# Optimization experiments

Hardware: AMD Instinct MI355X
Metric: run time of the kernel (lower is better)

## Reference

```python
import jax, jax.numpy as jnp
import numpy as np

NUM_HEAD = 8
HEAD_SIZE = 32  # attention_size 256 / 8 heads


def setup_inputs() -> dict:
    key = jax.random.key(0)
    ks = jax.random.split(key, 10)
    B, S, H, A = 2, 4096, 256, 256
    x = jax.random.normal(ks[0], (B, S, H), dtype=jnp.float32)
    mask = jax.random.randint(ks[1], (B, S), 0, 2) > 0  # bool key-padding mask
    s = 0.02
    wq = jax.random.normal(ks[2], (A, H), dtype=jnp.float32) * s
    bq = jax.random.normal(ks[3], (A,), dtype=jnp.float32) * s
    wk = jax.random.normal(ks[4], (A, H), dtype=jnp.float32) * s
    bk = jax.random.normal(ks[5], (A,), dtype=jnp.float32) * s
    wv = jax.random.normal(ks[6], (A, H), dtype=jnp.float32) * s
    bv = jax.random.normal(ks[7], (A,), dtype=jnp.float32) * s
    wo = jax.random.normal(ks[8], (H, A), dtype=jnp.float32) * s
    bo = jax.random.normal(ks[9], (H,), dtype=jnp.float32) * s
    return {"x": x, "mask": mask, "wq": wq, "bq": bq, "wk": wk, "bk": bk,
            "wv": wv, "bv": bv, "wo": wo, "bo": bo}


def reference(x, mask, wq, bq, wk, bk, wv, bv, wo, bo):
    B, S, _ = x.shape
    # QKV projections -> [B, S, n_head, head_size]
    q = (x @ wq.T + bq).reshape(B, S, NUM_HEAD, HEAD_SIZE)
    k = (x @ wk.T + bk).reshape(B, S, NUM_HEAD, HEAD_SIZE)
    v = (x @ wv.T + bv).reshape(B, S, NUM_HEAD, HEAD_SIZE)
    # scores [B, H, Sq, Sk]
    attn = jnp.einsum('bqhd,bkhd->bhqk', q, k) / jnp.sqrt(
        jnp.asarray(HEAD_SIZE, dtype=x.dtype))
    # attn*mask - 1e5*~mask  ==  where(mask, attn, -1e5)
    attn = jnp.where(mask[:, None, None, :], attn, jnp.asarray(-100000.0, dtype=x.dtype))
    p = jax.nn.softmax(attn, axis=-1)
    o = jnp.einsum('bhqk,bkhd->bqhd', p, v).reshape(B, S, NUM_HEAD * HEAD_SIZE)
    return o @ wo.T + bo
```

## Files before the change

### kernel.cpp

```cpp
#include <hip/hip_runtime.h>

#define DEV __device__ __forceinline__

typedef __attribute__((ext_vector_type(8)))  short bf16x8;
typedef __attribute__((ext_vector_type(4)))  short s16x4;
typedef __attribute__((ext_vector_type(16))) float f32x16;

constexpr int SB = 2;
constexpr int SS = 4096;
constexpr int SH = 256;
constexpr int NHEAD = 8, HD = 32;
constexpr int M_TOK = SB * SS;
constexpr int NQKV = 3 * SH;

constexpr size_t OFF_CNT  = 0;
constexpr size_t OFF_BIAS = 256;
constexpr size_t OFF_XB   = OFF_BIAS + 32768;
constexpr size_t OFF_WQKV = OFF_XB + (size_t)M_TOK * SH * 2;
constexpr size_t OFF_BQKV = OFF_WQKV + (size_t)NQKV * SH * 2;
constexpr size_t OFF_WOB  = OFF_BQKV + 4096;
constexpr size_t OFF_BO   = OFF_WOB + (size_t)SH * SH * 2;
constexpr size_t OFF_Q    = OFF_BO + 1024;
constexpr size_t OFF_K    = OFF_Q + (size_t)M_TOK * SH * 2;
constexpr size_t OFF_V    = OFF_K + (size_t)M_TOK * SH * 2;
constexpr size_t OFF_VT   = OFF_V + (size_t)M_TOK * SH * 2;
constexpr size_t OFF_O    = OFF_VT + (size_t)M_TOK * SH * 2;
constexpr size_t WS_NEED  = OFF_O + (size_t)M_TOK * SH * 2;

DEV short f2bf(float f) {
  unsigned u = __builtin_bit_cast(unsigned, f);
  u = (u + 0x7FFFu + ((u >> 16) & 1u)) >> 16;
  return (short)u;
}

DEV float bf2f(short s) {
  return __builtin_bit_cast(float, ((unsigned)(unsigned short)s) << 16);
}

DEV float exp2_(float x) {
#if __has_builtin(__builtin_amdgcn_exp2f)
  return __builtin_amdgcn_exp2f(x);
#else
  float r;
  asm("v_exp_f32 %0, %1\n\ts_nop 0" : "=v"(r) : "v"(x));
  return r;
#endif
}

DEV unsigned cvtpk(float lo, float hi) {
  unsigned r;
  asm("v_cvt_pk_bf16_f32 %0, %1, %2" : "=v"(r) : "v"(lo), "v"(hi));
  return r;
}

DEV void plswap(unsigned& a, unsigned& b) {
  asm("v_permlane32_swap_b32 %0, %1" : "+v"(a), "+v"(b));
}

__global__ void prep_kernel(const float* __restrict__ x,
    const float* __restrict__ wq, const float* __restrict__ bq,
    const float* __restrict__ wk, const float* __restrict__ bk,
    const float* __restrict__ wv, const float* __restrict__ bv,
    const float* __restrict__ wo, const float* __restrict__ bo,
    short* __restrict__ xb, short* __restrict__ Wqkv, float* __restrict__ bqkv,
    short* __restrict__ wob, float* __restrict__ bof) {
  const float QS = (float)(1.4426950408889634 / 5.656854249492381);
  long i = ((long)blockIdx.x * 256 + threadIdx.x) * 8;
  const long NX = (long)M_TOK * SH;
  const long NW = (long)NQKV * SH;
  if (i < NX) {
    const float4* s = (const float4*)(x + i);
    float4 f0 = s[0], f1 = s[1];
    bf16x8 o;
    o[0]=f2bf(f0.x); o[1]=f2bf(f0.y); o[2]=f2bf(f0.z); o[3]=f2bf(f0.w);
    o[4]=f2bf(f1.x); o[5]=f2bf(f1.y); o[6]=f2bf(f1.z); o[7]=f2bf(f1.w);
    *(bf16x8*)(xb + i) = o;
    return;
  }
  i -= NX;
  if (i < NW) {
    int n = (int)(i >> 8), kk = (int)(i & 255);
    int tn = n >> 8, rr = n & 255;
    const float* src = (tn == 0 ? wq : (tn == 1 ? wk : wv)) + rr * 256 + kk;
    float sc = tn == 0 ? QS : 1.f;
    float4 f0 = *(const float4*)src, f1 = *(const float4*)(src + 4);
    bf16x8 o;
    o[0]=f2bf(f0.x*sc); o[1]=f2bf(f0.y*sc); o[2]=f2bf(f0.z*sc); o[3]=f2bf(f0.w*sc);
    o[4]=f2bf(f1.x*sc); o[5]=f2bf(f1.y*sc); o[6]=f2bf(f1.z*sc); o[7]=f2bf(f1.w*sc);
    *(bf16x8*)(Wqkv + i) = o;
    return;
  }
  i -= NW;
  if (i < NQKV) {
    int n = (int)i;
#pragma unroll
    for (int j = 0; j < 8; ++j) {
      int nn = n + j, tn = nn >> 8, rr = nn & 255;
      const float* src = tn == 0 ? bq : (tn == 1 ? bk : bv);
      bqkv[nn] = src[rr] * (tn == 0 ? QS : 1.f);
    }
    return;
  }
  i -= NQKV;
  if (i < (long)SH * SH) {
    const float4* s = (const float4*)(wo + i);
    float4 f0 = s[0], f1 = s[1];
    bf16x8 o;
    o[0]=f2bf(f0.x); o[1]=f2bf(f0.y); o[2]=f2bf(f0.z); o[3]=f2bf(f0.w);
    o[4]=f2bf(f1.x); o[5]=f2bf(f1.y); o[6]=f2bf(f1.z); o[7]=f2bf(f1.w);
    *(bf16x8*)(wob + i) = o;
    return;
  }
  i -= (long)SH * SH;
  if (i < SH) {
#pragma unroll
    for (int j = 0; j < 8; ++j) bof[i + j] = bo[i + j];
  }
}

template <int MODE>
__global__ __launch_bounds__(256) void gemm_kernel(
    const short* __restrict__ Ag, const short* __restrict__ Bg,
    const float* __restrict__ bias,
    short* __restrict__ q, short* __restrict__ k, short* __restrict__ v,
    float* __restrict__ outf) {
  __shared__ __align__(16) short lA[8192];
  __shared__ __align__(16) short lB[4096];
  const int tid = threadIdx.x;
  const int lane = tid & 63, w = tid >> 6;
  const int wm = w >> 1, wn = w & 1;
  const int hi = lane >> 5, l31 = lane & 31;
  const int mb = blockIdx.x, nb = blockIdx.y;
  f32x16 acc0, acc1;
#pragma unroll
  for (int i = 0; i < 16; ++i) { acc0[i] = 0.f; acc1[i] = 0.f; }
  bf16x8 ra[4], rb[2];
  const int am = tid >> 3, ak = tid & 7;
  auto gload = [&](int kb) {
#pragma unroll
    for (int p = 0; p < 4; ++p)
      ra[p] = *(const bf16x8*)(Ag + (size_t)(mb * 128 + p * 32 + am) * 256 + kb * 64 + ak * 8);
#pragma unroll
    for (int p = 0; p < 2; ++p)
      rb[p] = *(const bf16x8*)(Bg + (size_t)(nb * 64 + p * 32 + am) * 256 + kb * 64 + ak * 8);
  };
  gload(0);
  for (int kb = 0; kb < 4; ++kb) {
    __syncthreads();
#pragma unroll
    for (int p = 0; p < 4; ++p)
      *(bf16x8*)(lA + (ak * 128 + p * 32 + am) * 8) = ra[p];
#pragma unroll
    for (int p = 0; p < 2; ++p)
      *(bf16x8*)(lB + (ak * 64 + p * 32 + am) * 8) = rb[p];
    __syncthreads();
    if (kb < 3) gload(kb + 1);
#pragma unroll
    for (int ks = 0; ks < 4; ++ks) {
      bf16x8 af0 = *(const bf16x8*)(lA + ((2 * ks + hi) * 128 + wm * 64 + l31) * 8);
      bf16x8 af1 = *(const bf16x8*)(lA + ((2 * ks + hi) * 128 + wm * 64 + 32 + l31) * 8);
      bf16x8 bf  = *(const bf16x8*)(lB + ((2 * ks + hi) * 64 + wn * 32 + l31) * 8);
      acc0 = __builtin_amdgcn_mfma_f32_32x32x16_bf16(af0, bf, acc0, 0, 0, 0);
      acc1 = __builtin_amdgcn_mfma_f32_32x32x16_bf16(af1, bf, acc1, 0, 0, 0);
    }
  }
  const int ncol = nb * 64 + wn * 32 + l31;
  const float bval = bias[ncol];
  if (MODE == 0) {
    const int tensor = nb >> 2;
    short* dst = tensor == 0 ? q : (tensor == 1 ? k : v);
    const int a = (nb & 3) * 64 + wn * 32 + l31;
    const int hh = a >> 5, d = a & 31;
#pragma unroll
    for (int mt = 0; mt < 2; ++mt) {
      const f32x16& acc = mt == 0 ? acc0 : acc1;
#pragma unroll
      for (int r = 0; r < 16; ++r) {
        int gm = mb * 128 + wm * 64 + mt * 32 + (r & 3) + 8 * (r >> 2) + 4 * hi;
        int bb = gm >> 12, ss = gm & 4095;
        dst[(((size_t)bb * NHEAD + hh) * SS + ss) * HD + d] = f2bf(acc[r] + bval);
      }
    }
  } else {
#pragma unroll
    for (int mt = 0; mt < 2; ++mt) {
      const f32x16& acc = mt == 0 ? acc0 : acc1;
#pragma unroll
      for (int r = 0; r < 16; ++r) {
        int gm = mb * 128 + wm * 64 + mt * 32 + (r & 3) + 8 * (r >> 2) + 4 * hi;
        outf[(size_t)gm * SH + ncol] = acc[r] + bval;
      }
    }
  }
}

__global__ void scan_mask_kernel(const unsigned char* __restrict__ m,
                                 int* __restrict__ idxC, float* __restrict__ biasC,
                                 int* __restrict__ cnts) {
  __shared__ int f_mis, f_off4, f_3f;
  __shared__ int ts[256];
  const int tid = threadIdx.x, b = blockIdx.x;
  if (tid == 0) { f_mis = 0; f_off4 = 0; f_3f = 0; }
  __syncthreads();
  int lm = 0, lo4 = 0, l3f = 0;
  for (int i = tid; i < 8192; i += 256) {
    unsigned char c = m[i];
    if (c) {
      if (i & 3) lm = 1;
      if ((i & 7) == 4) lo4 = 1;
      if ((i & 3) == 3 && c == 0x3F) l3f = 1;
    }
  }
  if (lm)  atomicOr(&f_mis, 1);
  if (lo4) atomicOr(&f_off4, 1);
  if (l3f) atomicOr(&f_3f, 1);
  __syncthreads();
  const int f = !f_mis ? (f_off4 ? 1 : 3) : (f_3f ? 2 : 0);
  int bits = 0;
  const int rbase = b * 4096 + tid * 16;
#pragma unroll
  for (int j = 0; j < 16; ++j) {
    int r = rbase + j;
    bool on;
    if (f == 0)      on = m[r] != 0;
    else if (f == 1) on = m[(size_t)r * 4] != 0;
    else if (f == 2) on = m[(size_t)r * 4 + 3] != 0;
    else             on = m[(size_t)r * 8] != 0;
    bits |= (int)on << j;
  }
  const int cnt = __popc(bits);
  ts[tid] = cnt;
  __syncthreads();
  for (int off = 1; off < 256; off <<= 1) {
    int u = (tid >= off) ? ts[tid - off] : 0;
    __syncthreads();
    ts[tid] += u;
    __syncthreads();
  }
  const int total = ts[255];
  int pos = ts[tid] - cnt;
  int* idxB = idxC + b * 4096;
  float* biasB = biasC + b * 4096;
  if (total == 0) {
    for (int j = tid; j < 4096; j += 256) { idxB[j] = j; biasB[j] = 0.f; }
    if (tid == 0) cnts[b] = 4096;
    return;
  }
#pragma unroll
  for (int j = 0; j < 16; ++j)
    if ((bits >> j) & 1) { idxB[pos] = tid * 16 + j; biasB[pos] = 0.f; ++pos; }
  int cntpad = (total + 255) & ~255;
  if (cntpad < 256) cntpad = 256;
  for (int j = total + tid; j < cntpad; j += 256) { idxB[j] = -1; biasB[j] = -100000.f; }
  if (tid == 0) cnts[b] = cntpad;
}

__global__ __launch_bounds__(256) void gather_kv_kernel(const short* __restrict__ K,
    const short* __restrict__ V, const int* __restrict__ idxC, const int* __restrict__ cnts,
    short* __restrict__ Kc, short* __restrict__ Vt) {
  const int bh = blockIdx.y, b = bh >> 3;
  const int jb = blockIdx.x * 64;
  if (jb >= cnts[b]) return;
  __shared__ short t[64][33];
  const int tid = threadIdx.x;
  const int s = tid >> 2, g = tid & 3;
  const int ix = idxC[b * 4096 + jb + s];
  bf16x8 kvv{}, vvv{};
  if (ix >= 0) {
    kvv = *(const bf16x8*)(K + ((size_t)bh * SS + ix) * HD + g * 8);
    vvv = *(const bf16x8*)(V + ((size_t)bh * SS + ix) * HD + g * 8);
  }
  *(bf16x8*)(Kc + ((size_t)bh * SS + jb + s) * HD + g * 8) = kvv;
#pragma unroll
  for (int j = 0; j < 8; ++j) t[s][g * 8 + j] = vvv[j];
  __syncthreads();
  const int d = tid >> 3, gs = tid & 7;
  bf16x8 out;
#pragma unroll
  for (int j = 0; j < 8; ++j) out[j] = t[gs * 8 + j][d];
  *(bf16x8*)(Vt + ((size_t)bh * HD + d) * SS + jb + gs * 8) = out;
}

__global__ __launch_bounds__(256, 4) void attn_kernel(const short* __restrict__ Q,
    const short* __restrict__ Kc, const short* __restrict__ Vt,
    const float* __restrict__ biasC, const int* __restrict__ cnts,
    short* __restrict__ OP0, short* __restrict__ OP1, float* __restrict__ Lp) {
  __shared__ __align__(16) short sK[4096];
  __shared__ __align__(16) short sV[4096];
  __shared__ __align__(16) float sB[128];
  const int tid = threadIdx.x;
  const int lane = tid & 63, wave = tid >> 6;
  const int hi = lane >> 5, l31 = lane & 31;
  const int qblk = blockIdx.x, bh = blockIdx.y, half = blockIdx.z;
  const int b = bh >> 3, h = bh & 7;
  const int Lh = cnts[b] >> 1;
  const int NIT = Lh >> 7;
  const int kv0 = half * Lh;
  const short* Kb = Kc + ((size_t)bh * SS + kv0) * HD;
  const short* Vb = Vt + (size_t)bh * HD * SS + kv0;
  const float* biasB = biasC + b * SS + kv0;
  const int qbase = qblk * 128 + wave * 32;
  const short* Qrow = Q + ((size_t)bh * SS + qbase + l31) * HD;
  const bf16x8 qf0 = *(const bf16x8*)(Qrow + hi * 8);
  const bf16x8 qf1 = *(const bf16x8*)(Qrow + 16 + hi * 8);
  bf16x8 ones;
#pragma unroll
  for (int j = 0; j < 8; ++j) ones[j] = (short)0x3F80;
  f32x16 accO, lacc;
#pragma unroll
  for (int i = 0; i < 16; ++i) { accO[i] = 0.f; lacc[i] = 0.f; }
  const int kvs = tid >> 2, gd = tid & 3;
  const int dv = tid >> 3, gkv = tid & 7;
  const short* kvsrc = Kb + (size_t)kvs * HD + gd * 8;
  const short* vvsrc = Vb + (size_t)dv * SS + gkv * 8;
  short* kdst0 = sK + ((size_t)gd * 128 + kvs) * 8;
  short* kdst1 = sK + ((size_t)gd * 128 + 64 + kvs) * 8;
  short* vdst0 = sV + ((size_t)gkv * 32 + dv) * 8;
  short* vdst1 = sV + ((size_t)(gkv + 8) * 32 + dv) * 8;
  bf16x8 stgK0 = *(const bf16x8*)kvsrc;
  bf16x8 stgK1 = *(const bf16x8*)(kvsrc + 64 * HD);
  bf16x8 stgV0 = *(const bf16x8*)vvsrc;
  bf16x8 stgV1 = *(const bf16x8*)(vvsrc + 64);
  float stgb = (tid < 128) ? biasB[tid] : 0.f;

  for (int kt = 0; kt < NIT; ++kt) {
    __syncthreads();
    *(bf16x8*)kdst0 = stgK0;
    *(bf16x8*)kdst1 = stgK1;
    *(bf16x8*)vdst0 = stgV0;
    *(bf16x8*)vdst1 = stgV1;
    if (tid < 128) sB[tid] = stgb;
    __syncthreads();
    if (kt + 1 < NIT) {
      const short* ks = kvsrc + (size_t)(kt + 1) * 128 * HD;
      stgK0 = *(const bf16x8*)ks;
      stgK1 = *(const bf16x8*)(ks + 64 * HD);
      const short* vs = vvsrc + (kt + 1) * 128;
      stgV0 = *(const bf16x8*)vs;
      stgV1 = *(const bf16x8*)(vs + 64);
      if (tid < 128) stgb = biasB[(kt + 1) * 128 + tid];
    }
#pragma unroll
    for (int sub = 0; sub < 2; ++sub) {
      const int kb = sub * 64;
      const float4* bp4 = (const float4*)(sB + kb);
      f32x16 s0, s1;
#pragma unroll
      for (int qd = 0; qd < 4; ++qd) {
        float4 f0 = bp4[2 * qd + hi];
        float4 f1 = bp4[8 + 2 * qd + hi];
        s0[4 * qd + 0] = f0.x; s0[4 * qd + 1] = f0.y; s0[4 * qd + 2] = f0.z; s0[4 * qd + 3] = f0.w;
        s1[4 * qd + 0] = f1.x; s1[4 * qd + 1] = f1.y; s1[4 * qd + 2] = f1.z; s1[4 * qd + 3] = f1.w;
      }
      const bf16x8 a00 = *(const bf16x8*)(sK + ((hi)*128 + kb + l31) * 8);
      const bf16x8 a01 = *(const bf16x8*)(sK + ((2 + hi) * 128 + kb + l31) * 8);
      const bf16x8 a10 = *(const bf16x8*)(sK + ((hi)*128 + kb + 32 + l31) * 8);
      const bf16x8 a11 = *(const bf16x8*)(sK + ((2 + hi) * 128 + kb + 32 + l31) * 8);
      s0 = __builtin_amdgcn_mfma_f32_32x32x16_bf16(a00, qf0, s0, 0, 0, 0);
      s0 = __builtin_amdgcn_mfma_f32_32x32x16_bf16(a01, qf1, s0, 0, 0, 0);
      s1 = __builtin_amdgcn_mfma_f32_32x32x16_bf16(a10, qf0, s1, 0, 0, 0);
      s1 = __builtin_amdgcn_mfma_f32_32x32x16_bf16(a11, qf1, s1, 0, 0, 0);
      f32x16 p;
#pragma unroll
      for (int r = 0; r < 16; ++r) p[r] = exp2_(s0[r]);
      bf16x8 pa1, pa2;
      {
        unsigned a0 = cvtpk(p[0], p[1]),   a1 = cvtpk(p[2], p[3]);
        unsigned b0 = cvtpk(p[4], p[5]),   b1 = cvtpk(p[6], p[7]);
        plswap(a0, b0); plswap(a1, b1);
        unsigned c0 = cvtpk(p[8], p[9]),   c1 = cvtpk(p[10], p[11]);
        unsigned d0 = cvtpk(p[12], p[13]), d1 = cvtpk(p[14], p[15]);
        plswap(c0, d0); plswap(c1, d1);
        union { unsigned u[4]; bf16x8 v; } x, y;
        x.u[0] = a0; x.u[1] = a1; x.u[2] = b0; x.u[3] = b1;
        y.u[0] = c0; y.u[1] = c1; y.u[2] = d0; y.u[3] = d1;
        pa1 = x.v; pa2 = y.v;
      }
      const bf16x8 vb0 = *(const bf16x8*)(sV + ((sub * 8 + hi) * 32 + l31) * 8);
      const bf16x8 vb1 = *(const bf16x8*)(sV + ((sub * 8 + 2 + hi) * 32 + l31) * 8);
      accO = __builtin_amdgcn_mfma_f32_32x32x16_bf16(pa1, vb0, accO, 0, 0, 0);
      accO = __builtin_amdgcn_mfma_f32_32x32x16_bf16(pa2, vb1, accO, 0, 0, 0);
      lacc = __builtin_amdgcn_mfma_f32_32x32x16_bf16(pa1, ones, lacc, 0, 0, 0);
      lacc = __builtin_amdgcn_mfma_f32_32x32x16_bf16(pa2, ones, lacc, 0, 0, 0);
#pragma unroll
      for (int r = 0; r < 16; ++r) p[r] = exp2_(s1[r]);
      bf16x8 pa3, pa4;
      {
        unsigned a0 = cvtpk(p[0], p[1]),   a1 = cvtpk(p[2], p[3]);
        unsigned b0 = cvtpk(p[4], p[5]),   b1 = cvtpk(p[6], p[7]);
        plswap(a0, b0); plswap(a1, b1);
        unsigned c0 = cvtpk(p[8], p[9]),   c1 = cvtpk(p[10], p[11]);
        unsigned d0 = cvtpk(p[12], p[13]), d1 = cvtpk(p[14], p[15]);
        plswap(c0, d0); plswap(c1, d1);
        union { unsigned u[4]; bf16x8 v; } x, y;
        x.u[0] = a0; x.u[1] = a1; x.u[2] = b0; x.u[3] = b1;
        y.u[0] = c0; y.u[1] = c1; y.u[2] = d0; y.u[3] = d1;
        pa3 = x.v; pa4 = y.v;
      }
      const bf16x8 vb2 = *(const bf16x8*)(sV + ((sub * 8 + 4 + hi) * 32 + l31) * 8);
      const bf16x8 vb3 = *(const bf16x8*)(sV + ((sub * 8 + 6 + hi) * 32 + l31) * 8);
      accO = __builtin_amdgcn_mfma_f32_32x32x16_bf16(pa3, vb2, accO, 0, 0, 0);
      accO = __builtin_amdgcn_mfma_f32_32x32x16_bf16(pa4, vb3, accO, 0, 0, 0);
      lacc = __builtin_amdgcn_mfma_f32_32x32x16_bf16(pa3, ones, lacc, 0, 0, 0);
      lacc = __builtin_amdgcn_mfma_f32_32x32x16_bf16(pa4, ones, lacc, 0, 0, 0);
    }
  }
  short* OP = half ? OP1 : OP0;
#pragma unroll
  for (int r = 0; r < 16; ++r) {
    int qq = (r & 3) + 8 * (r >> 2) + 4 * hi;
    int m = b * SS + qbase + qq;
    OP[(size_t)m * SH + h * HD + l31] = f2bf(accO[r]);
    if (l31 == 0) Lp[((size_t)half * 16 + bh) * SS + qbase + qq] = lacc[r];
  }
}

__global__ __launch_bounds__(256) void combine_kernel(const short* __restrict__ P0,
    const short* __restrict__ P1, const float* __restrict__ Lp,
    short* __restrict__ Ow) {
  int t = blockIdx.x * 256 + threadIdx.x;
  int m = t >> 6, c4 = (t & 63) * 4;
  int b = m >> 12, s = m & 4095, h = c4 >> 5;
  s16x4 o0 = *(const s16x4*)(P0 + (size_t)m * SH + c4);
  s16x4 o1 = *(const s16x4*)(P1 + (size_t)m * SH + c4);
  int bh = b * 8 + h;
  float l = Lp[(size_t)bh * SS + s] + Lp[((size_t)16 + bh) * SS + s];
  float rcp = 1.f / l;
  s16x4 out;
#pragma unroll
  for (int j = 0; j < 4; ++j) out[j] = f2bf((bf2f(o0[j]) + bf2f(o1[j])) * rcp);
  *(s16x4*)(Ow + (size_t)m * SH + c4) = out;
}

extern "C" void kernel_launch(void* const* d_in, const int* in_sizes, int n_in,
                              void* d_out, int out_size, void* d_ws, size_t ws_size,
                              hipStream_t stream) {
  (void)in_sizes; (void)n_in; (void)out_size;
  if (ws_size < WS_NEED) return;
  const float* x  = (const float*)d_in[0];
  const unsigned char* mask = (const unsigned char*)d_in[1];
  const float* wq = (const float*)d_in[2];
  const float* bq = (const float*)d_in[3];
  const float* wk = (const float*)d_in[4];
  const float* bk = (const float*)d_in[5];
  const float* wv = (const float*)d_in[6];
  const float* bv = (const float*)d_in[7];
  const float* wo = (const float*)d_in[8];
  const float* bo = (const float*)d_in[9];
  char* ws = (char*)d_ws;
  int*   cnts    = (int*)(ws + OFF_CNT);
  short* xb      = (short*)(ws + OFF_XB);
  short* Wqkv    = (short*)(ws + OFF_WQKV);
  float* bqkv    = (float*)(ws + OFF_BQKV);
  short* wob     = (short*)(ws + OFF_WOB);
  float* bof     = (float*)(ws + OFF_BO);
  short* Qw      = (short*)(ws + OFF_Q);
  short* Kw      = (short*)(ws + OFF_K);
  short* Vw      = (short*)(ws + OFF_V);
  short* Vtw     = (short*)(ws + OFF_VT);
  short* Kc      = (short*)(ws + OFF_XB);
  int*   idxC    = (int*)(ws + OFF_WQKV);
  float* biasC   = (float*)(ws + OFF_WQKV + 65536);
  short* OP0     = (short*)(ws + OFF_K);
  short* OP1     = (short*)(ws + OFF_V);
  float* Lp      = (float*)(ws + OFF_O);

  prep_kernel<<<1153, 256, 0, stream>>>(x, wq, bq, wk, bk, wv, bv, wo, bo,
                                        xb, Wqkv, bqkv, wob, bof);
  gemm_kernel<0><<<dim3(64, 12), 256, 0, stream>>>(xb, Wqkv, bqkv, Qw, Kw, Vw, nullptr);
  scan_mask_kernel<<<2, 256, 0, stream>>>(mask, idxC, biasC, cnts);
  gather_kv_kernel<<<dim3(64, 16), 256, 0, stream>>>(Kw, Vw, idxC, cnts, Kc, Vtw);
  attn_kernel<<<dim3(32, 16, 2), 256, 0, stream>>>(Qw, Kc, Vtw, biasC, cnts, OP0, OP1, Lp);
  combine_kernel<<<2048, 256, 0, stream>>>(OP0, OP1, Lp, OP0);
  gemm_kernel<1><<<dim3(64, 4), 256, 0, stream>>>(OP0, wob, bof,
                                                  nullptr, nullptr, nullptr, (float*)d_out);
}
```

Before: 90.46 us.

## Split exp2 between hardware transcendental and polynomial emulation; remap KV staging threads

Half of the softmax exponentials now use a cubic polynomial with exponent bit manipulation on the regular VALU, while the other half keep the hardware v_exp_f32. The aim is to spread the exponential work so the transcendental unit does not bottleneck the attention inner loop. Separately, the thread-to-element mapping for staging K and V tiles into shared memory is changed so consecutive threads write consecutive LDS rows, which may reduce bank conflicts or change global coalescing. The polynomial adds some approximation error and extra VALU instructions.

Measured after the change: 99.62 us. 10.1% more time.

```diff
diff --git a/kernel.cpp b/kernel.cpp
--- a/kernel.cpp
+++ b/kernel.cpp
@@ -45,6 +45,18 @@
   asm("v_exp_f32 %0, %1\n\ts_nop 0" : "=v"(r) : "v"(x));
   return r;
 #endif
+}
+
+DEV float fexp2(float s) {
+  s = fmaxf(s, -125.0f);
+  float fl = __builtin_floorf(s);
+  float f = s - fl;
+  float p = 0.0792043f;
+  p = p * f + 0.2243384f;
+  p = p * f + 0.6964573f;
+  p = p * f + 0.9998930f;
+  int ib = (int)fl;
+  return __builtin_bit_cast(float, __builtin_bit_cast(int, p) + (ib << 23));
 }
 
 DEV unsigned cvtpk(float lo, float hi) {
@@ -309,14 +321,14 @@
   f32x16 accO, lacc;
 #pragma unroll
   for (int i = 0; i < 16; ++i) { accO[i] = 0.f; lacc[i] = 0.f; }
-  const int kvs = tid >> 2, gd = tid & 3;
-  const int dv = tid >> 3, gkv = tid & 7;
-  const short* kvsrc = Kb + (size_t)kvs * HD + gd * 8;
-  const short* vvsrc = Vb + (size_t)dv * SS + gkv * 8;
-  short* kdst0 = sK + ((size_t)gd * 128 + kvs) * 8;
-  short* kdst1 = sK + ((size_t)gd * 128 + 64 + kvs) * 8;
-  short* vdst0 = sV + ((size_t)gkv * 32 + dv) * 8;
-  short* vdst1 = sV + ((size_t)(gkv + 8) * 32 + dv) * 8;
+  const int kgd = tid >> 6, kkv = tid & 63;
+  const int vdv = tid & 31, vgk = tid >> 5;
+  const short* kvsrc = Kb + (size_t)kkv * HD + kgd * 8;
+  const short* vvsrc = Vb + (size_t)vdv * SS + vgk * 8;
+  short* kdst0 = sK + ((size_t)kgd * 128 + kkv) * 8;
+  short* kdst1 = kdst0 + 64 * 8;
+  short* vdst0 = sV + ((size_t)vgk * 32 + vdv) * 8;
+  short* vdst1 = vdst0 + 8 * 32 * 8;
   bf16x8 stgK0 = *(const bf16x8*)kvsrc;
   bf16x8 stgK1 = *(const bf16x8*)(kvsrc + 64 * HD);
   bf16x8 stgV0 = *(const bf16x8*)vvsrc;
@@ -362,7 +374,7 @@
       s1 = __builtin_amdgcn_mfma_f32_32x32x16_bf16(a11, qf1, s1, 0, 0, 0);
       f32x16 p;
 #pragma unroll
-      for (int r = 0; r < 16; ++r) p[r] = exp2_(s0[r]);
+      for (int r = 0; r < 16; ++r) p[r] = (r & 1) ? fexp2(s0[r]) : exp2_(s0[r]);
       bf16x8 pa1, pa2;
       {
         unsigned a0 = cvtpk(p[0], p[1]),   a1 = cvtpk(p[2], p[3]);
@@ -383,7 +395,7 @@
       lacc = __builtin_amdgcn_mfma_f32_32x32x16_bf16(pa1, ones, lacc, 0, 0, 0);
       lacc = __builtin_amdgcn_mfma_f32_32x32x16_bf16(pa2, ones, lacc, 0, 0, 0);
 #pragma unroll
-      for (int r = 0; r < 16; ++r) p[r] = exp2_(s1[r]);
+      for (int r = 0; r < 16; ++r) p[r] = (r & 1) ? fexp2(s1[r]) : exp2_(s1[r]);
       bf16x8 pa3, pa4;
       {
         unsigned a0 = cvtpk(p[0], p[1]),   a1 = cvtpk(p[2], p[3]);
```
